# Optimization experiments

Hardware: AMD Instinct MI355X
Metric: run time of the kernel (lower is better)

The kernel has to match this reference:

```python
import jax, jax.numpy as jnp
import numpy as np

H = 1152  # hidden_size
NH = 16   # num_attention_heads
HD = H // NH  # head_dim = 72
FF = 4304  # intermediate_size
EPS = 1e-6
S = 4096
B = 1
NDOCS = 32


def _linear_params(key, d_in, d_out):
    kw, kb = jax.random.split(key)
    lim = 1.0 / np.sqrt(d_in)
    w = jax.random.uniform(kw, (d_out, d_in), jnp.float32, -lim, lim)
    b = jax.random.uniform(kb, (d_out,), jnp.float32, -lim, lim)
    return w, b


def setup_inputs() -> dict:
    key = jax.random.key(0)
    ks = jax.random.split(key, 8)
    hidden_states = jax.random.normal(ks[0], (B, S, H), jnp.float32)
    document_ids = jnp.sort(jax.random.randint(ks[1], (S,), 0, NDOCS))
    q_w, q_b = _linear_params(ks[2], H, H)
    k_w, k_b = _linear_params(ks[3], H, H)
    v_w, v_b = _linear_params(ks[4], H, H)
    o_w, o_b = _linear_params(ks[5], H, H)
    fc1_w, fc1_b = _linear_params(ks[6], H, FF)
    fc2_w, fc2_b = _linear_params(ks[7], FF, H)
    return {
        'hidden_states': hidden_states,
        'document_ids': document_ids,
        'q_w': q_w, 'q_b': q_b, 'k_w': k_w, 'k_b': k_b,
        'v_w': v_w, 'v_b': v_b, 'o_w': o_w, 'o_b': o_b,
        'ln1_g': jnp.ones((H,), jnp.float32), 'ln1_b': jnp.zeros((H,), jnp.float32),
        'ln2_g': jnp.ones((H,), jnp.float32), 'ln2_b': jnp.zeros((H,), jnp.float32),
        'fc1_w': fc1_w, 'fc1_b': fc1_b, 'fc2_w': fc2_w, 'fc2_b': fc2_b,
    }


def _layer_norm(x, g, b):
    mu = jnp.mean(x, axis=-1, keepdims=True)
    var = jnp.mean(jnp.square(x - mu), axis=-1, keepdims=True)
    return (x - mu) * jax.lax.rsqrt(var + EPS) * g + b


def _forward(hidden_states, q_w, q_b, k_w, k_b, v_w, v_b, o_w, o_b,
             ln1_g, ln1_b, ln2_g, ln2_b, fc1_w, fc1_b, fc2_w, fc2_b,
             document_ids):
    b, s, _ = hidden_states.shape
    scale = HD ** -0.5

    residual = hidden_states
    x = _layer_norm(hidden_states, ln1_g, ln1_b)

    # projections (torch Linear: y = x @ W.T + b)
    q = (x @ q_w.T + q_b).reshape(b, s, NH, HD).transpose(0, 2, 1, 3)
    k = (x @ k_w.T + k_b).reshape(b, s, NH, HD).transpose(0, 2, 1, 3)
    v = (x @ v_w.T + v_b).reshape(b, s, NH, HD).transpose(0, 2, 1, 3)

    # document-masked attention: attend only within same document id
    scores = jnp.einsum('bhqd,bhkd->bhqk', q, k) * scale
    mask = document_ids[:, None] == document_ids[None, :]  # [s, s]
    scores = jnp.where(mask[None, None], scores, -jnp.inf)
    attn = jax.nn.softmax(scores, axis=-1)
    out = jnp.einsum('bhqk,bhkd->bhqd', attn, v)  # [b,h,s,d]
    out = out.transpose(0, 2, 1, 3).reshape(b, s, H)
    out = out @ o_w.T + o_b

    hidden = residual + out
    residual = hidden
    x = _layer_norm(hidden, ln2_g, ln2_b)
    x = jax.nn.gelu(x @ fc1_w.T + fc1_b, approximate=True)
    x = x @ fc2_w.T + fc2_b
    return residual + x


def reference(hidden_states, document_ids, q_w, q_b, k_w, k_b, v_w, v_b,
              o_w, o_b, ln1_g, ln1_b, ln2_g, ln2_b, fc1_w, fc1_b, fc2_w, fc2_b):
    return _forward(hidden_states, q_w, q_b, k_w, k_b, v_w, v_b, o_w, o_b,
                    ln1_g, ln1_b, ln2_g, ln2_b, fc1_w, fc1_b, fc2_w, fc2_b,
                    document_ids)
```

## Files before the change

kernel.cpp:

```cpp
#include <hip/hip_runtime.h>

typedef unsigned short u16;
typedef unsigned int u32;
typedef __attribute__((ext_vector_type(8))) __bf16 bf16x8;
typedef __attribute__((ext_vector_type(8))) u16 u16x8;
typedef __attribute__((ext_vector_type(4))) float f32x4;
typedef __attribute__((ext_vector_type(2))) u32 u32x2;

#define SEQ 4096
#define HID 1152
#define NHEAD 16
#define HDIM 72
#define FF 4304
#define FFP 4352
#define H3 3456

__device__ __forceinline__ u16 f2bf(float f) {
  u32 u = __builtin_bit_cast(u32, f);
  u32 r = u + 0x7fffu + ((u >> 16) & 1u);
  return (u16)(r >> 16);
}
__device__ __forceinline__ float bf2f(u16 h) {
  return __builtin_bit_cast(float, (u32)h << 16);
}
__device__ __forceinline__ float bflo(u32 u) { return __builtin_bit_cast(float, u << 16); }
__device__ __forceinline__ float bfhi(u32 u) { return __builtin_bit_cast(float, u & 0xffff0000u); }

typedef const __attribute__((address_space(1))) void* gas_t;
typedef __attribute__((address_space(3))) void* las_t;
__device__ __forceinline__ void load_lds16(const void* g, void* l) {
  __builtin_amdgcn_global_load_lds((gas_t)(unsigned long long)g,
                                   (las_t)(u32)(unsigned long long)l, 16, 0, 0);
}

__device__ __forceinline__ float gelu_fast(float x) {
  float z = 0.7978845608f * (x + 0.044715f * x * x * x);
  return x / (1.f + __expf(-2.f * z));
}

__global__ __launch_bounds__(256) void cvt4x4_k(const float* __restrict__ a,
                                                const float* __restrict__ b,
                                                const float* __restrict__ c,
                                                const float* __restrict__ d,
                                                u16* __restrict__ out, int n4) {
  int i = blockIdx.x * 256 + threadIdx.x;
  if (i >= n4) return;
  const float* in = (blockIdx.y == 0) ? a : (blockIdx.y == 1) ? b : (blockIdx.y == 2) ? c : d;
  f32x4 f = ((const f32x4*)in)[i];
  u32x2 o;
  o[0] = (u32)f2bf(f[0]) | ((u32)f2bf(f[1]) << 16);
  o[1] = (u32)f2bf(f[2]) | ((u32)f2bf(f[3]) << 16);
  ((u32x2*)(out + (size_t)blockIdx.y * n4 * 4))[i] = o;
}

__global__ __launch_bounds__(256) void cvt4_pad_k(const float* __restrict__ in,
                                                  u16* __restrict__ out,
                                                  int rows, int sc, int dc) {
  int i = blockIdx.x * 256 + threadIdx.x;
  long long n4 = (long long)rows * dc / 4;
  if (i >= n4) return;
  long long idx = (long long)i * 4;
  int r = (int)(idx / dc);
  int c = (int)(idx % dc);
  u32x2 o;
  if (c < sc) {
    f32x4 f = *(const f32x4*)(in + (size_t)r * sc + c);
    o[0] = (u32)f2bf(f[0]) | ((u32)f2bf(f[1]) << 16);
    o[1] = (u32)f2bf(f[2]) | ((u32)f2bf(f[3]) << 16);
  } else {
    o[0] = 0; o[1] = 0;
  }
  ((u32x2*)out)[i] = o;
}

__global__ __launch_bounds__(256) void prep_k(const int* __restrict__ ids,
                                              const float* __restrict__ qb,
                                              const float* __restrict__ kb,
                                              const float* __restrict__ vb,
                                              const float* __restrict__ f1b,
                                              int* __restrict__ se,
                                              float* __restrict__ bqkv,
                                              float* __restrict__ bf1,
                                              float* __restrict__ zbuf) {
  int i = blockIdx.x * 256 + threadIdx.x;
  if (i < H3) bqkv[i] = (i < HID) ? qb[i] : (i < 2 * HID ? kb[i - HID] : vb[i - 2 * HID]);
  if (i < FFP) bf1[i] = (i < FF) ? f1b[i] : 0.f;
  if (i < 16) zbuf[i] = 0.f;
  if (i < SEQ) {
    int id = ids[i];
    int lo = 0, hi = SEQ;
    while (lo < hi) { int mid = (lo + hi) >> 1; if (ids[mid] < id) lo = mid + 1; else hi = mid; }
    int s = lo;
    lo = 0; hi = SEQ;
    while (lo < hi) { int mid = (lo + hi) >> 1; if (ids[mid] <= id) lo = mid + 1; else hi = mid; }
    se[2 * i] = s;
    se[2 * i + 1] = lo;
  }
}

__global__ __launch_bounds__(256) void ln_k(const float* __restrict__ x,
                                            const float* __restrict__ g,
                                            const float* __restrict__ b,
                                            u16* __restrict__ y) {
  __shared__ float sred[8];
  int row = blockIdx.x, tid = threadIdx.x;
  const f32x4* xr = (const f32x4*)(x + (size_t)row * HID);
  f32x4 v0 = {}, v1 = {};
  float s = 0.f, s2 = 0.f;
  int c0 = tid, c1 = tid + 256;
  v0 = xr[c0];
  if (c1 < 288) v1 = xr[c1];
#pragma unroll
  for (int j = 0; j < 4; ++j) { s += v0[j] + v1[j]; s2 += v0[j] * v0[j] + v1[j] * v1[j]; }
#pragma unroll
  for (int sh = 32; sh; sh >>= 1) { s += __shfl_xor(s, sh); s2 += __shfl_xor(s2, sh); }
  if ((tid & 63) == 0) { sred[tid >> 6] = s; sred[4 + (tid >> 6)] = s2; }
  __syncthreads();
  s = sred[0] + sred[1] + sred[2] + sred[3];
  s2 = sred[4] + sred[5] + sred[6] + sred[7];
  float mu = s * (1.f / HID);
  float rs = rsqrtf(s2 * (1.f / HID) - mu * mu + 1e-6f);
  u16* yr = y + (size_t)row * HID;
  const f32x4* g4 = (const f32x4*)g;
  const f32x4* b4 = (const f32x4*)b;
  {
    f32x4 gv = g4[c0], bv = b4[c0];
    u32x2 o;
    o[0] = (u32)f2bf((v0[0] - mu) * rs * gv[0] + bv[0]) |
           ((u32)f2bf((v0[1] - mu) * rs * gv[1] + bv[1]) << 16);
    o[1] = (u32)f2bf((v0[2] - mu) * rs * gv[2] + bv[2]) |
           ((u32)f2bf((v0[3] - mu) * rs * gv[3] + bv[3]) << 16);
    *(u32x2*)(yr + c0 * 4) = o;
  }
  if (c1 < 288) {
    f32x4 gv = g4[c1], bv = b4[c1];
    u32x2 o;
    o[0] = (u32)f2bf((v1[0] - mu) * rs * gv[0] + bv[0]) |
           ((u32)f2bf((v1[1] - mu) * rs * gv[1] + bv[1]) << 16);
    o[1] = (u32)f2bf((v1[2] - mu) * rs * gv[2] + bv[2]) |
           ((u32)f2bf((v1[3] - mu) * rs * gv[3] + bv[3]) << 16);
    *(u32x2*)(yr + c1 * 4) = o;
  }
}

template <int EP>
__global__ __launch_bounds__(256, 2) void gemm_bt(const u16* __restrict__ A,
                                                  const u16* __restrict__ B,
                                                  void* __restrict__ outp,
                                                  const float* __restrict__ bias,
                                                  const float* __restrict__ resid,
                                                  int M, int N, int K) {
  __shared__ u16 As[128 * 64];
  __shared__ u16 Bs[128 * 64];
  int tid = threadIdx.x;
  int l = tid & 63, w = tid >> 6;
  int nxy = gridDim.x * gridDim.y;
  int bidf = blockIdx.y * gridDim.x + blockIdx.x;
  int cpx = nxy >> 3;
  bidf = (bidf & 7) * cpx + (bidf >> 3);
  int m0 = (bidf / gridDim.x) * 128;
  int n0 = (bidf % gridDim.x) * 128;
  int wr = w >> 1, wc = w & 1;
  f32x4 acc[4][4] = {};
  int srow = tid >> 3;
  int scol = ((tid & 7) * 16) ^ ((srow & 7) << 4);
  const char* Ab = (const char*)A + ((size_t)(m0 + srow) * K) * 2 + scol;
  const char* Bb = (const char*)B + ((size_t)(n0 + srow) * K) * 2 + scol;
  char* AsD = (char*)As + w * 1024;
  char* BsD = (char*)Bs + w * 1024;
  const char* ArB = (const char*)As + (wr * 64 + (l & 15)) * 128;
  const char* BrB = (const char*)Bs + (wc * 64 + (l & 15)) * 128;
  int c0 = ((l >> 4) * 16) ^ ((l & 7) << 4);
  int c1 = c0 ^ 64;
  int k0 = 0, kend = K;
  if (EP == 5) {
    int nz = gridDim.z;
    int ksp = ((K / 64 + nz - 1) / nz) * 64;
    k0 = blockIdx.z * ksp;
    kend = min(K, k0 + ksp);
  }
  for (int kt = k0; kt < kend; kt += 64) {
    size_t kb = (size_t)kt * 2;
#pragma unroll
    for (int i = 0; i < 4; ++i) {
      load_lds16(Ab + (size_t)i * 32 * K * 2 + kb, AsD + i * 4096);
      load_lds16(Bb + (size_t)i * 32 * K * 2 + kb, BsD + i * 4096);
    }
    __syncthreads();
#pragma unroll
    for (int kk = 0; kk < 2; ++kk) {
      int ck = kk ? c1 : c0;
      bf16x8 af[4], bfr[4];
#pragma unroll
      for (int m = 0; m < 4; ++m) af[m] = *(const bf16x8*)(ArB + m * 2048 + ck);
#pragma unroll
      for (int n = 0; n < 4; ++n) bfr[n] = *(const bf16x8*)(BrB + n * 2048 + ck);
#pragma unroll
      for (int m = 0; m < 4; ++m)
#pragma unroll
        for (int n = 0; n < 4; ++n)
          acc[m][n] = __builtin_amdgcn_mfma_f32_16x16x32_bf16(af[m], bfr[n], acc[m][n], 0, 0, 0);
    }
    __syncthreads();
  }
#pragma unroll
  for (int m = 0; m < 4; ++m) {
    int row = m0 + wr * 64 + m * 16 + (l >> 4) * 4;
#pragma unroll
    for (int n = 0; n < 4; ++n) {
      int col = n0 + wc * 64 + n * 16 + (l & 15);
      float bv = (EP == 5) ? 0.f : bias[col];
      if (EP == 4) {
        int region = (col >= 2304) ? 2 : (col >= 1152 ? 1 : 0);
        int cw = col - region * 1152;
        int hh = cw / 72;
        int dd = cw - hh * 72;
        u16* dst = (u16*)outp + (((size_t)region * NHEAD + hh) * SEQ) * HDIM + dd;
#pragma unroll
        for (int j = 0; j < 4; ++j)
          dst[(size_t)(row + j) * HDIM] = f2bf(acc[m][n][j] + bv);
      } else if (EP == 5) {
        u16* P = (u16*)outp + (size_t)blockIdx.z * M * N;
#pragma unroll
        for (int j = 0; j < 4; ++j)
          P[(size_t)(row + j) * N + col] = f2bf(acc[m][n][j]);
      } else {
#pragma unroll
        for (int j = 0; j < 4; ++j) {
          size_t idx = (size_t)(row + j) * N + col;
          float v = acc[m][n][j] + bv;
          if (EP == 1) ((u16*)outp)[idx] = f2bf(gelu_fast(v));
          else ((float*)outp)[idx] = v + resid[idx];
        }
      }
    }
  }
}

template <int NS>
__global__ __launch_bounds__(256) void splitk_reduce_k(const u16* __restrict__ P,
                                                       const float* __restrict__ bias,
                                                       const float* __restrict__ resid,
                                                       float* __restrict__ out, int n4) {
  int i = blockIdx.x * 256 + threadIdx.x;
  if (i >= n4) return;
  size_t base = (size_t)i * 4;
  int col = (int)(base % HID);
  f32x4 a = {};
#pragma unroll
  for (int s = 0; s < NS; ++s) {
    u32x2 pv = *(const u32x2*)(P + (size_t)s * SEQ * HID + base);
    a[0] += bflo(pv[0]);
    a[1] += bfhi(pv[0]);
    a[2] += bflo(pv[1]);
    a[3] += bfhi(pv[1]);
  }
  f32x4 bv = *(const f32x4*)(bias + col);
  f32x4 rv = ((const f32x4*)resid)[i];
  ((f32x4*)out)[i] = a + bv + rv;
}

__device__ __forceinline__ u32 swz(u32 a) { return a ^ (((a >> 8) & 7u) << 4); }

__global__ __launch_bounds__(256, 2) void attn_mfma_k(const u16* __restrict__ qkvh,
                                                      const int* __restrict__ se,
                                                      const float* __restrict__ zb,
                                                      u16* __restrict__ outb) {
  __shared__ u16 Ks[128 * 104];
  __shared__ u16 Vt[80 * 128];
  __shared__ u16 Ps[4][16 * 128];
  __shared__ int Sq[64], Eq[64];
  int tid = threadIdx.x, l = tid & 63, w = tid >> 6;
  int h = blockIdx.y, q0 = blockIdx.x * 64;
  const float scale = 0.1178511302f;
  const u16* Qh = qkvh + (size_t)h * SEQ * HDIM;
  const u16* Kh = qkvh + ((size_t)NHEAD + h) * SEQ * HDIM;
  const u16* Vh = qkvh + ((size_t)2 * NHEAD + h) * SEQ * HDIM;

  for (int i = tid; i < 512; i += 256) ((u32*)(Vt + 72 * 128))[i] = 0;

#pragma unroll
  for (int it = 0; it < 4; ++it) {
    int cw0 = it * 256 + w * 64;
    if (cw0 < 832) {
      int chunk = cw0 + l;
      int row = chunk / 13, c16 = chunk - row * 13;
      const void* src = (c16 < 9)
                            ? (const void*)(Qh + ((size_t)(q0 + row)) * HDIM + c16 * 8)
                            : (const void*)zb;
      load_lds16(src, (char*)Ks + (size_t)cw0 * 16);
    }
  }
  if (tid < 64) { Sq[tid] = se[2 * (q0 + tid)]; Eq[tid] = se[2 * (q0 + tid) + 1]; }
  __syncthreads();

  int sqj[4], eqj[4];
#pragma unroll
  for (int j = 0; j < 4; ++j) {
    int ql = w * 16 + (l >> 4) * 4 + j;
    sqj[j] = Sq[ql]; eqj[j] = Eq[ql];
  }
  const char* Aq = (const char*)Ks + (w * 16 + (l & 15)) * 208 + (l >> 4) * 16;
  bf16x8 aq[3];
#pragma unroll
  for (int dsl = 0; dsl < 3; ++dsl) aq[dsl] = *(const bf16x8*)(Aq + dsl * 64);
  __syncthreads();

  int kmin = se[2 * q0];
  int kmax = se[2 * (q0 + 63) + 1];
  f32x4 o[5] = {};
  float m_run[4], l_run[4];
#pragma unroll
  for (int j = 0; j < 4; ++j) { m_run[j] = -1e30f; l_run[j] = 0.f; }

  for (int kc = kmin; kc < kmax; kc += 128) {
#pragma unroll
    for (int it = 0; it < 7; ++it) {
      int cw0 = it * 256 + w * 64;
      if (cw0 < 1664) {
        int chunk = cw0 + l;
        int row = chunk / 13, c16 = chunk - row * 13;
        int krow = kc + row;
        const void* src = (c16 < 9 && krow < SEQ)
                              ? (const void*)(Kh + (size_t)krow * HDIM + c16 * 8)
                              : (const void*)zb;
        load_lds16(src, (char*)Ks + (size_t)cw0 * 16);
      }
    }
#pragma unroll
    for (int it = 0; it < 3; ++it) {
      int idx = it * 256 + tid;
      if (idx < 576) {
        int k2 = idx / 9, d8 = idx - k2 * 9;
        int kr0 = kc + 2 * k2, kr1 = kr0 + 1;
        kr0 = kr0 < SEQ ? kr0 : SEQ - 1;
        kr1 = kr1 < SEQ ? kr1 : SEQ - 1;
        u16x8 r0 = *(const u16x8*)(Vh + (size_t)kr0 * HDIM + d8 * 8);
        u16x8 r1 = *(const u16x8*)(Vh + (size_t)kr1 * HDIM + d8 * 8);
#pragma unroll
        for (int j = 0; j < 8; ++j) {
          u32 pr = (u32)r0[j] | ((u32)r1[j] << 16);
          *(u32*)((char*)Vt + swz((u32)(d8 * 8 + j) * 256 + (u32)k2 * 4)) = pr;
        }
      }
    }
    __syncthreads();

    f32x4 sf[8];
#pragma unroll
    for (int kt = 0; kt < 8; ++kt) {
      const char* Bk = (const char*)Ks + (kt * 16 + (l & 15)) * 208 + (l >> 4) * 16;
      f32x4 acc = {};
      acc = __builtin_amdgcn_mfma_f32_16x16x32_bf16(aq[0], *(const bf16x8*)Bk, acc, 0, 0, 0);
      acc = __builtin_amdgcn_mfma_f32_16x16x32_bf16(aq[1], *(const bf16x8*)(Bk + 64), acc, 0, 0, 0);
      acc = __builtin_amdgcn_mfma_f32_16x16x32_bf16(aq[2], *(const bf16x8*)(Bk + 128), acc, 0, 0, 0);
      sf[kt] = acc;
    }
    float mx[4] = {-1e30f, -1e30f, -1e30f, -1e30f};
#pragma unroll
    for (int kt = 0; kt < 8; ++kt) {
      int key = kc + kt * 16 + (l & 15);
#pragma unroll
      for (int j = 0; j < 4; ++j) {
        float s = sf[kt][j] * scale;
        bool valid = (key >= sqj[j]) && (key < eqj[j]);
        s = valid ? s : -1e30f;
        sf[kt][j] = s;
        mx[j] = fmaxf(mx[j], s);
      }
    }
#pragma unroll
    for (int j = 0; j < 4; ++j) {
      float m = mx[j];
      m = fmaxf(m, __shfl_xor(m, 1));
      m = fmaxf(m, __shfl_xor(m, 2));
      m = fmaxf(m, __shfl_xor(m, 4));
      m = fmaxf(m, __shfl_xor(m, 8));
      mx[j] = m;
    }
    float fz[4], ps[4];
#pragma unroll
    for (int j = 0; j < 4; ++j) {
      float mn = fmaxf(m_run[j], mx[j]);
      fz[j] = __expf(m_run[j] - mn);
      m_run[j] = mn;
      ps[j] = 0.f;
    }
#pragma unroll
    for (int kt = 0; kt < 8; ++kt)
#pragma unroll
      for (int j = 0; j < 4; ++j) {
        float s = sf[kt][j];
        float p = (s > -1e29f) ? __expf(s - m_run[j]) : 0.f;
        sf[kt][j] = p;
        ps[j] += p;
      }
#pragma unroll
    for (int j = 0; j < 4; ++j) {
      float p = ps[j];
      p += __shfl_xor(p, 1);
      p += __shfl_xor(p, 2);
      p += __shfl_xor(p, 4);
      p += __shfl_xor(p, 8);
      l_run[j] = l_run[j] * fz[j] + p;
#pragma unroll
      for (int dt = 0; dt < 5; ++dt) o[dt][j] *= fz[j];
    }
    char* PB = (char*)Ps[w];
#pragma unroll
    for (int kt = 0; kt < 8; ++kt)
#pragma unroll
      for (int j = 0; j < 4; ++j) {
        u32 a = (u32)((l >> 4) * 4 + j) * 256 + (u32)(kt * 16 + (l & 15)) * 2;
        *(u16*)(PB + swz(a)) = f2bf(sf[kt][j]);
      }
#pragma unroll
    for (int ks = 0; ks < 4; ++ks) {
      u32 aa = (u32)(l & 15) * 256 + (u32)((l >> 4) * 8 + ks * 32) * 2;
      bf16x8 ap = *(const bf16x8*)(PB + swz(aa));
#pragma unroll
      for (int dt = 0; dt < 5; ++dt) {
        u32 ba = (u32)(dt * 16 + (l & 15)) * 256 + (u32)((l >> 4) * 8 + ks * 32) * 2;
        bf16x8 bv = *(const bf16x8*)((const char*)Vt + swz(ba));
        o[dt] = __builtin_amdgcn_mfma_f32_16x16x32_bf16(ap, bv, o[dt], 0, 0, 0);
      }
    }
    __syncthreads();
  }

  float inv[4];
#pragma unroll
  for (int j = 0; j < 4; ++j) inv[j] = 1.f / l_run[j];
#pragma unroll
  for (int dt = 0; dt < 5; ++dt) {
    int d = dt * 16 + (l & 15);
    if (d < HDIM) {
#pragma unroll
      for (int j = 0; j < 4; ++j) {
        int q = q0 + w * 16 + (l >> 4) * 4 + j;
        outb[(size_t)q * HID + h * HDIM + d] = f2bf(o[dt][j] * inv[j]);
      }
    }
  }
}

constexpr size_t SZ_WQKV = (size_t)H3 * HID * 2;
constexpr size_t SZ_WO   = (size_t)HID * HID * 2;
constexpr size_t SZ_WF1  = (size_t)FFP * HID * 2;
constexpr size_t SZ_WF2  = (size_t)HID * FFP * 2;
constexpr size_t OFF_WQKV = 0;
constexpr size_t OFF_WO   = OFF_WQKV + SZ_WQKV;
constexpr size_t OFF_WF1  = OFF_WO + SZ_WO;
constexpr size_t OFF_BQKV = OFF_WF1 + SZ_WF1;
constexpr size_t OFF_BF1  = OFF_BQKV + (size_t)H3 * 4;
constexpr size_t OFF_SE   = OFF_BF1 + (size_t)FFP * 4;
constexpr size_t OFF_ZB   = OFF_SE + (size_t)SEQ * 2 * 4;
constexpr size_t OFF_XLN  = OFF_ZB + 64;
constexpr size_t OFF_QKV  = OFF_XLN + (size_t)SEQ * HID * 2;
constexpr size_t OFF_ACT  = OFF_QKV;
constexpr size_t OFF_AOUT = OFF_QKV + (size_t)SEQ * H3 * 2;
constexpr size_t OFF_HD   = OFF_AOUT + (size_t)SEQ * HID * 2;
constexpr size_t OFF_WF2  = OFF_HD + (size_t)SEQ * HID * 4;
constexpr size_t WS_NEED  = OFF_WF2 + SZ_WF2;
constexpr size_t OFF_P    = 0;
static_assert(OFF_ACT + (size_t)SEQ * FFP * 2 <= OFF_HD, "ACT must not clobber HD");
static_assert(3 * (size_t)SEQ * HID * 2 <= OFF_QKV, "P must stay in dead prefix");

extern "C" void kernel_launch(void* const* d_in, const int* in_sizes, int n_in,
                              void* d_out, int out_size, void* d_ws, size_t ws_size,
                              hipStream_t stream) {
  const float* hs   = (const float*)d_in[0];
  const int*   ids  = (const int*)d_in[1];
  const float* q_w  = (const float*)d_in[2];
  const float* q_b  = (const float*)d_in[3];
  const float* k_w  = (const float*)d_in[4];
  const float* k_b  = (const float*)d_in[5];
  const float* v_w  = (const float*)d_in[6];
  const float* v_b  = (const float*)d_in[7];
  const float* o_w  = (const float*)d_in[8];
  const float* o_b  = (const float*)d_in[9];
  const float* ln1g = (const float*)d_in[10];
  const float* ln1b = (const float*)d_in[11];
  const float* ln2g = (const float*)d_in[12];
  const float* ln2b = (const float*)d_in[13];
  const float* f1w  = (const float*)d_in[14];
  const float* f1b  = (const float*)d_in[15];
  const float* f2w  = (const float*)d_in[16];
  const float* f2b  = (const float*)d_in[17];

  if (ws_size < WS_NEED) return;

  char* ws = (char*)d_ws;
  u16*   Wqkv = (u16*)(ws + OFF_WQKV);
  u16*   Wf1  = (u16*)(ws + OFF_WF1);
  u16*   Wf2  = (u16*)(ws + OFF_WF2);
  float* Bqkv = (float*)(ws + OFF_BQKV);
  float* Bf1  = (float*)(ws + OFF_BF1);
  int*   SE   = (int*)(ws + OFF_SE);
  float* ZB   = (float*)(ws + OFF_ZB);
  u16*   XLN  = (u16*)(ws + OFF_XLN);
  u16*   QKVh = (u16*)(ws + OFF_QKV);
  u16*   ACT  = (u16*)(ws + OFF_ACT);
  u16*   AOUT = (u16*)(ws + OFF_AOUT);
  float* HD   = (float*)(ws + OFF_HD);
  u16*   Pp   = (u16*)(ws + OFF_P);
  u16*   Wo   = (u16*)(ws + OFF_WO);

  prep_k<<<dim3((FFP + 255) / 256), dim3(256), 0, stream>>>(ids, q_b, k_b, v_b, f1b, SE, Bqkv,
                                                            Bf1, ZB);
  int nW = HID * HID;
  cvt4x4_k<<<dim3(nW / 4 / 256, 4), dim3(256), 0, stream>>>(q_w, k_w, v_w, o_w, Wqkv, nW / 4);
  {
    int n4 = FFP * HID / 4;
    cvt4_pad_k<<<dim3((n4 + 255) / 256), dim3(256), 0, stream>>>(f1w, Wf1, 1, FF * HID, FFP * HID);
  }
  {
    int n4 = HID * FFP / 4;
    cvt4_pad_k<<<dim3((n4 + 255) / 256), dim3(256), 0, stream>>>(f2w, Wf2, HID, FF, FFP);
  }

  ln_k<<<dim3(SEQ), dim3(256), 0, stream>>>(hs, ln1g, ln1b, XLN);
  gemm_bt<4><<<dim3(H3 / 128, SEQ / 128), dim3(256), 0, stream>>>(XLN, Wqkv, QKVh, Bqkv, nullptr,
                                                                  SEQ, H3, HID);
  attn_mfma_k<<<dim3(SEQ / 64, NHEAD), dim3(256), 0, stream>>>(QKVh, SE, ZB, AOUT);
  gemm_bt<2><<<dim3(HID / 128, SEQ / 128), dim3(256), 0, stream>>>(AOUT, Wo, HD, o_b, hs,
                                                                   SEQ, HID, HID);
  ln_k<<<dim3(SEQ), dim3(256), 0, stream>>>(HD, ln2g, ln2b, XLN);
  gemm_bt<1><<<dim3(FFP / 128, SEQ / 128), dim3(256), 0, stream>>>(XLN, Wf1, ACT, Bf1, nullptr,
                                                                   SEQ, FFP, HID);
  gemm_bt<5><<<dim3(HID / 128, SEQ / 128, 3), dim3(256), 0, stream>>>(ACT, Wf2, Pp, nullptr,
                                                                      nullptr, SEQ, HID, FFP);
  splitk_reduce_k<3><<<dim3(SEQ * HID / 4 / 256), dim3(256), 0, stream>>>(Pp, f2b, HD,
                                                                          (float*)d_out,
                                                                          SEQ * HID / 4);
}
```

Baseline: 293.0 us.

## Double-buffer LDS tiles in GEMM to overlap global loads with MFMA

Doubles the shared-memory A/B tile buffers in the bf16 GEMM kernel so the next K-step tile is prefetched while the current tile is used for MFMA. Manual vmcnt waits and raw s_barrier calls replace the __syncthreads pairs, letting outstanding loads stay in flight across the compute. This doubles LDS usage to 64KB per block, which may limit occupancy under the 2-blocks launch bound, and it depends on vmcnt counting being correct for the direct-to-LDS loads.

```diff
diff --git a/kernel.cpp b/kernel.cpp
--- a/kernel.cpp
+++ b/kernel.cpp
@@ -150,8 +150,8 @@
                                                   const float* __restrict__ bias,
                                                   const float* __restrict__ resid,
                                                   int M, int N, int K) {
-  __shared__ u16 As[128 * 64];
-  __shared__ u16 Bs[128 * 64];
+  __shared__ u16 As[2 * 128 * 64];
+  __shared__ u16 Bs[2 * 128 * 64];
   int tid = threadIdx.x;
   int l = tid & 63, w = tid >> 6;
   int nxy = gridDim.x * gridDim.y;
@@ -166,10 +166,8 @@
   int scol = ((tid & 7) * 16) ^ ((srow & 7) << 4);
   const char* Ab = (const char*)A + ((size_t)(m0 + srow) * K) * 2 + scol;
   const char* Bb = (const char*)B + ((size_t)(n0 + srow) * K) * 2 + scol;
-  char* AsD = (char*)As + w * 1024;
-  char* BsD = (char*)Bs + w * 1024;
-  const char* ArB = (const char*)As + (wr * 64 + (l & 15)) * 128;
-  const char* BrB = (const char*)Bs + (wc * 64 + (l & 15)) * 128;
+  int rowA = (wr * 64 + (l & 15)) * 128;
+  int rowB = (wc * 64 + (l & 15)) * 128;
   int c0 = ((l >> 4) * 16) ^ ((l & 7) << 4);
   int c1 = c0 ^ 64;
   int k0 = 0, kend = K;
@@ -179,29 +177,53 @@
     k0 = blockIdx.z * ksp;
     kend = min(K, k0 + ksp);
   }
-  for (int kt = k0; kt < kend; kt += 64) {
-    size_t kb = (size_t)kt * 2;
+  int nsteps = (kend - k0) / 64;
+  char* cA = (char*)As;
+  char* nA = (char*)As + 16384;
+  char* cB = (char*)Bs;
+  char* nB = (char*)Bs + 16384;
+  {
+    size_t kb = (size_t)k0 * 2;
 #pragma unroll
     for (int i = 0; i < 4; ++i) {
-      load_lds16(Ab + (size_t)i * 32 * K * 2 + kb, AsD + i * 4096);
-      load_lds16(Bb + (size_t)i * 32 * K * 2 + kb, BsD + i * 4096);
-    }
-    __syncthreads();
+      load_lds16(Ab + (size_t)i * 32 * K * 2 + kb, cA + w * 1024 + i * 4096);
+      load_lds16(Bb + (size_t)i * 32 * K * 2 + kb, cB + w * 1024 + i * 4096);
+    }
+  }
+  for (int s = 0; s < nsteps; ++s) {
+    if (s + 1 < nsteps) {
+      size_t kb = (size_t)(k0 + (s + 1) * 64) * 2;
+#pragma unroll
+      for (int i = 0; i < 4; ++i) {
+        load_lds16(Ab + (size_t)i * 32 * K * 2 + kb, nA + w * 1024 + i * 4096);
+        load_lds16(Bb + (size_t)i * 32 * K * 2 + kb, nB + w * 1024 + i * 4096);
+      }
+      asm volatile("s_waitcnt vmcnt(8)" ::: "memory");
+    } else {
+      asm volatile("s_waitcnt vmcnt(0)" ::: "memory");
+    }
+    __builtin_amdgcn_s_barrier();
+    __builtin_amdgcn_sched_barrier(0);
 #pragma unroll
     for (int kk = 0; kk < 2; ++kk) {
       int ck = kk ? c1 : c0;
       bf16x8 af[4], bfr[4];
 #pragma unroll
-      for (int m = 0; m < 4; ++m) af[m] = *(const bf16x8*)(ArB + m * 2048 + ck);
-#pragma unroll
-      for (int n = 0; n < 4; ++n) bfr[n] = *(const bf16x8*)(BrB + n * 2048 + ck);
+      for (int m = 0; m < 4; ++m) af[m] = *(const bf16x8*)(cA + rowA + m * 2048 + ck);
+#pragma unroll
+      for (int n = 0; n < 4; ++n) bfr[n] = *(const bf16x8*)(cB + rowB + n * 2048 + ck);
 #pragma unroll
       for (int m = 0; m < 4; ++m)
 #pragma unroll
         for (int n = 0; n < 4; ++n)
           acc[m][n] = __builtin_amdgcn_mfma_f32_16x16x32_bf16(af[m], bfr[n], acc[m][n], 0, 0, 0);
     }
-    __syncthreads();
+    __builtin_amdgcn_sched_barrier(0);
+    __builtin_amdgcn_s_barrier();
+    __builtin_amdgcn_sched_barrier(0);
+    char* t;
+    t = cA; cA = nA; nA = t;
+    t = cB; cB = nB; nB = t;
   }
 #pragma unroll
   for (int m = 0; m < 4; ++m) {
```

New measurement: 289.1 us. Within noise of the previous version (-1.3%).
